# Performance work log

Measured on AMD Instinct MI355X. Metric: run time of the kernel, lower is better.

## Reference

```python
import jax, jax.numpy as jnp
import numpy as np

B, N, C = 8, 1024, 1024
H = 16
D = C // H  # head_dim = 64


def apply_rope(t, cos, sin):
    # t: (B,H,N,D), cos/sin: (N, D//2). Interleaved-pair RoPE
    # (matches repeat_interleave(2) + stack(-y2,y1) in the torch code).
    tr = t.reshape(*t.shape[:-1], D // 2, 2)
    t1, t2 = tr[..., 0], tr[..., 1]
    o1 = t1 * cos - t2 * sin
    o2 = t2 * cos + t1 * sin
    return jnp.stack((o1, o2), axis=-1).reshape(t.shape)


def setup_inputs() -> dict:
    key = jax.random.key(0)
    k1, k2, k3, k4 = jax.random.split(key, 4)
    s = 0.02
    x = jax.random.normal(k1, (B, N, C), dtype=jnp.float32)
    w_qkv = jax.random.normal(k2, (C, 3 * C), dtype=jnp.float32) * s  # qkv_bias=False
    w_proj = jax.random.normal(k3, (C, C), dtype=jnp.float32) * s
    b_proj = jax.random.normal(k4, (C,), dtype=jnp.float32) * s
    return {"x": x, "w_qkv": w_qkv, "w_proj": w_proj, "b_proj": b_proj}


def reference(x, w_qkv, w_proj, b_proj):
    # QKV projection: (B,N,3C) -> (3,B,H,N,D)
    qkv = (x @ w_qkv).reshape(B, N, 3, H, D).transpose(2, 0, 3, 1, 4)
    q, k, v = qkv[0], qkv[1], qkv[2]

    # RoPE tables: pos = arange(N) (mask=None, no cls/registers)
    pos = jnp.arange(N, dtype=jnp.float32)
    omega = 1.0 / (10000.0 ** (jnp.arange(D // 2, dtype=jnp.float32) / (D / 2.0)))
    freq = pos[:, None] * omega  # (N, D//2)
    cos, sin = jnp.cos(freq), jnp.sin(freq)

    q = apply_rope(q, cos, sin)
    k = apply_rope(k, cos, sin)

    # Scaled dot-product attention (non-causal, no dropout in eval)
    scale = 1.0 / jnp.sqrt(jnp.float32(D))
    scores = jnp.einsum('bhqd,bhkd->bhqk', q, k) * scale
    attn = jax.nn.softmax(scores, axis=-1)
    out = jnp.einsum('bhqk,bhkd->bhqd', attn, v)

    # Merge heads + output projection
    out = out.transpose(0, 2, 1, 3).reshape(B, N, C)
    return out @ w_proj + b_proj
```

## Files before the change

kernel.cpp:

```cpp
#include <hip/hip_runtime.h>
#include <hip/hip_bf16.h>
#include <math.h>

#define Bsz  8
#define Nseq 1024
#define Cdim 1024
#define Hh   16
#define Dd   64

typedef short short8 __attribute__((ext_vector_type(8)));
typedef float floatx4 __attribute__((ext_vector_type(4)));

__device__ __forceinline__ unsigned short f2bf(float f) {
    __hip_bfloat16 h = __float2bfloat16(f);
    return __builtin_bit_cast(unsigned short, h);
}
__device__ __forceinline__ float b2f(unsigned short u) {
    return __uint_as_float(((unsigned)u) << 16);
}

__device__ __forceinline__ void async16(const void* g, void* l) {
    __builtin_amdgcn_global_load_lds(
        (const __attribute__((address_space(1))) unsigned int*)g,
        (__attribute__((address_space(3))) unsigned int*)l, 16, 0, 0);
}

__device__ __forceinline__ unsigned pack_bf16(float lo, float hi) {
    unsigned ulo = __float_as_uint(lo) + 0x8000u;
    unsigned uhi = __float_as_uint(hi) + 0x8000u;
    return __builtin_amdgcn_perm(uhi, ulo, 0x07060302);
}

__global__ __launch_bounds__(256) void prep(
    const float* __restrict__ x, const float* __restrict__ w_qkv,
    const float* __restrict__ w_proj,
    unsigned short* __restrict__ xb, unsigned short* __restrict__ wqkvt,
    unsigned short* __restrict__ wprojt, float2* __restrict__ rope)
{
    __shared__ float T[64][65];
    const int blk = blockIdx.x;
    const int tid = threadIdx.x;

    if (blk < 8192) {
        int i = blk * 256 + tid;
        float4 v = ((const float4*)x)[i];
        ushort4 u;
        u.x = f2bf(v.x); u.y = f2bf(v.y); u.z = f2bf(v.z); u.w = f2bf(v.w);
        ((ushort4*)xb)[i] = u;
        return;
    }
    if (blk < 9216) {
        const float* in;
        unsigned short* out;
        int R = 1024, Ccols, c0, r0;
        if (blk < 8960) {
            int b2 = blk - 8192;
            in = w_qkv; out = wqkvt; Ccols = 3072;
            c0 = (b2 % 48) * 64; r0 = (b2 / 48) * 64;
        } else {
            int b2 = blk - 8960;
            in = w_proj; out = wprojt; Ccols = 1024;
            c0 = (b2 % 16) * 64; r0 = (b2 / 16) * 64;
        }
        for (int i = tid; i < 4096; i += 256) {
            int r = i >> 6, c = i & 63;
            T[r][c] = in[(size_t)(r0 + r) * Ccols + c0 + c];
        }
        __syncthreads();
        for (int i = tid; i < 4096; i += 256) {
            int rr = i >> 6, cc = i & 63;
            out[(size_t)(c0 + rr) * R + r0 + cc] = f2bf(T[cc][rr]);
        }
        return;
    }
    {
        int i = (blk - 9216) * 256 + tid;
        int n = i >> 5, p = i & 31;
        float omega = __expf(-(float)p * 0.2878231366242557f);
        float sv, cv;
        sincosf((float)n * omega, &sv, &cv);
        rope[i] = make_float2(cv, sv);
    }
}

template <int MODE>
__global__ __launch_bounds__(256) void gemm_bf16(
    const unsigned short* __restrict__ A, const unsigned short* __restrict__ Bt,
    const float* __restrict__ bias, const float2* __restrict__ rope,
    unsigned short* __restrict__ qb, unsigned short* __restrict__ kb,
    unsigned short* __restrict__ vtb, float* __restrict__ out)
{
    const int K = 1024;
    __shared__ short SM[2][128][64];
    const int tid  = threadIdx.x;
    const int wave = tid >> 6, lane = tid & 63;
    const int ml = lane & 15, quad = lane >> 4;
    const int wm = wave >> 1, wn = wave & 1;
    const int bm = blockIdx.y * 128, bn = blockIdx.x * 128;

    const int lr     = lane >> 3;
    const int lchunk = ((lane & 7) ^ lr) * 8;

    floatx4 acc[4][4] = {};

    for (int k0 = 0; k0 < K; k0 += 64) {
        #pragma unroll
        for (int t = 0; t < 4; ++t) {
            int r8  = (wave * 4 + t) * 8;
            int row = r8 + lr;
            async16(A  + (size_t)(bm + row) * K + k0 + lchunk, &SM[0][r8][0]);
            async16(Bt + (size_t)(bn + row) * K + k0 + lchunk, &SM[1][r8][0]);
        }
        __syncthreads();

        #pragma unroll
        for (int ks = 0; ks < 2; ++ks) {
            const int sl = ((ks * 4 + quad) ^ (ml & 7)) * 8;
            short8 araw[4], braw[4];
            #pragma unroll
            for (int mi = 0; mi < 4; ++mi)
                araw[mi] = *(const short8*)&SM[0][wm * 64 + mi * 16 + ml][sl];
            #pragma unroll
            for (int ni = 0; ni < 4; ++ni)
                braw[ni] = *(const short8*)&SM[1][wn * 64 + ni * 16 + ml][sl];
            #pragma unroll
            for (int mi = 0; mi < 4; ++mi)
                #pragma unroll
                for (int ni = 0; ni < 4; ++ni)
                    acc[mi][ni] = __builtin_amdgcn_mfma_f32_16x16x32_bf16(
                        araw[mi], braw[ni], acc[mi][ni], 0, 0, 0);
        }
        __syncthreads();
    }

    if (MODE == 0) {
        const int region = bn >> 10;
        const int b = bm >> 10;
        if (region < 2) {
            float2* Rs = (float2*)&SM[0][0][0];
            #pragma unroll
            for (int t = 0; t < 16; ++t) {
                int idx = t * 256 + tid;
                Rs[idx] = rope[(size_t)((bm + (idx >> 5)) & 1023) * 32 + (idx & 31)];
            }
            __syncthreads();
            unsigned short* dst = (region == 0) ? qb : kb;
            const float scale = (region == 0) ? 0.125f : 1.f;
            const float sgn = (ml & 1) ? 1.f : -1.f;
            #pragma unroll
            for (int ni = 0; ni < 4; ++ni) {
                int col = bn + wn * 64 + ni * 16 + ml;
                int jj = col & 1023;
                int h = jj >> 6, d = jj & 63;
                int p = d >> 1;
                #pragma unroll
                for (int mi = 0; mi < 4; ++mi)
                    #pragma unroll
                    for (int r = 0; r < 4; ++r) {
                        int rl = wm * 64 + mi * 16 + quad * 4 + r;
                        int n  = (bm + rl) & 1023;
                        float val = acc[mi][ni][r];
                        float partner = __shfl_xor(val, 1);
                        float2 cs = Rs[rl * 32 + p];
                        dst[(((size_t)(b * Hh + h)) * Nseq + n) * Dd + d] =
                            f2bf((val * cs.x + sgn * partner * cs.y) * scale);
                    }
            }
        } else {
            short* T = &SM[0][0][0];
            const int n0 = bm & 1023;
            #pragma unroll
            for (int hw = 0; hw < 2; ++hw) {
                if (hw) __syncthreads();
                if (wn == hw) {
                    #pragma unroll
                    for (int ni = 0; ni < 4; ++ni) {
                        int dcol = ni * 16 + ml;
                        #pragma unroll
                        for (int mi = 0; mi < 4; ++mi)
                            #pragma unroll
                            for (int r = 0; r < 4; ++r) {
                                int rl = wm * 64 + mi * 16 + quad * 4 + r;
                                T[dcol * 132 + rl] = (short)f2bf(acc[mi][ni][r]);
                            }
                    }
                }
                __syncthreads();
                int h = ((bn & 1023) >> 6) + hw;
                #pragma unroll
                for (int t = 0; t < 8; ++t) {
                    int idx4 = t * 256 + tid;
                    int d = idx4 >> 5, seg = idx4 & 31;
                    ushort4 v4 = *(const ushort4*)&T[d * 132 + seg * 4];
                    *(ushort4*)(vtb + (((size_t)(b * Hh + h)) * Dd + d) * Nseq
                                + n0 + seg * 4) = v4;
                }
            }
        }
    } else {
        #pragma unroll
        for (int ni = 0; ni < 4; ++ni) {
            int col = bn + wn * 64 + ni * 16 + ml;
            float bv = bias[col];
            #pragma unroll
            for (int mi = 0; mi < 4; ++mi)
                #pragma unroll
                for (int r = 0; r < 4; ++r) {
                    int row = bm + wm * 64 + mi * 16 + quad * 4 + r;
                    out[(size_t)row * 1024 + col] = acc[mi][ni][r] + bv;
                }
        }
    }
}

__global__ __launch_bounds__(256) void attn_flash_mfma(
    const unsigned short* __restrict__ qb, const unsigned short* __restrict__ kb,
    const unsigned short* __restrict__ vt, unsigned short* __restrict__ ao)
{
    const int bh  = blockIdx.x;
    const int qt  = blockIdx.y;
    const int tid = threadIdx.x;
    const int wave = tid >> 6, lane = tid & 63;
    const int ml = lane & 15, quad = lane >> 4;
    const int lr = lane >> 3;
    const int lc = ((lane & 7) ^ lr) * 8;

    __shared__ short Qs[128][64];
    __shared__ short Ks[64][64];
    __shared__ short Vs[64][64];
    __shared__ short Ps[4][32][72];

    const size_t hbase = (size_t)bh * (Nseq * Dd);
    const size_t vbase = (size_t)bh * 64;
    const int q0 = qt * 128;
    const int wq = wave * 32;
    const int wk = wave * 16;

    #pragma unroll
    for (int t = 0; t < 4; ++t)
        async16(qb + hbase + (size_t)(q0 + wq + t * 8 + lr) * 64 + lc, &Qs[wq + t * 8][0]);
    async16(kb + hbase + (size_t)(wk + lr) * 64 + lc,     &Ks[wk][0]);
    async16(kb + hbase + (size_t)(wk + 8 + lr) * 64 + lc, &Ks[wk + 8][0]);
    __syncthreads();

    short8 qfr[2][2];
    #pragma unroll
    for (int ks = 0; ks < 2; ++ks) {
        const int sl = ((ks * 4 + quad) ^ (ml & 7)) * 8;
        qfr[ks][0] = *(const short8*)&Qs[wq + ml][sl];
        qfr[ks][1] = *(const short8*)&Qs[wq + 16 + ml][sl];
    }

    float l0 = 0.f, l1 = 0.f;
    floatx4 o[2][4] = {};

    for (int kt = 0; kt < 16; ++kt) {
        const int k0r = kt * 64;
        async16(vt + (vbase + wk + lr) * Nseq + k0r + lc,     &Vs[wk][0]);
        async16(vt + (vbase + wk + 8 + lr) * Nseq + k0r + lc, &Vs[wk + 8][0]);

        floatx4 st[2][4] = {};
        #pragma unroll
        for (int ks = 0; ks < 2; ++ks) {
            const int sl = ((ks * 4 + quad) ^ (ml & 7)) * 8;
            #pragma unroll
            for (int kbk = 0; kbk < 4; ++kbk) {
                short8 kf = *(const short8*)&Ks[kbk * 16 + ml][sl];
                st[0][kbk] = __builtin_amdgcn_mfma_f32_16x16x32_bf16(kf, qfr[ks][0], st[0][kbk], 0, 0, 0);
                st[1][kbk] = __builtin_amdgcn_mfma_f32_16x16x32_bf16(kf, qfr[ks][1], st[1][kbk], 0, 0, 0);
            }
        }

        #pragma unroll
        for (int qg = 0; qg < 2; ++qg) {
            float lacc = 0.f;
            #pragma unroll
            for (int kbk = 0; kbk < 4; ++kbk) {
                float e0 = __expf(st[qg][kbk][0]);
                float e1 = __expf(st[qg][kbk][1]);
                float e2 = __expf(st[qg][kbk][2]);
                float e3 = __expf(st[qg][kbk][3]);
                lacc += (e0 + e1) + (e2 + e3);
                uint2 pk;
                pk.x = pack_bf16(e0, e1);
                pk.y = pack_bf16(e2, e3);
                *(uint2*)&Ps[wave][qg * 16 + ml][kbk * 16 + quad * 4] = pk;
            }
            if (qg == 0) l0 += lacc; else l1 += lacc;
        }
        __syncthreads();

        if (kt < 15) {
            const int k1r = k0r + 64;
            async16(kb + hbase + (size_t)(k1r + wk + lr) * 64 + lc,     &Ks[wk][0]);
            async16(kb + hbase + (size_t)(k1r + wk + 8 + lr) * 64 + lc, &Ks[wk + 8][0]);
        }

        #pragma unroll
        for (int ks = 0; ks < 2; ++ks) {
            const int sl = ((ks * 4 + quad) ^ (ml & 7)) * 8;
            short8 pf0 = *(const short8*)&Ps[wave][ml][ks * 32 + quad * 8];
            short8 pf1 = *(const short8*)&Ps[wave][16 + ml][ks * 32 + quad * 8];
            #pragma unroll
            for (int nt = 0; nt < 4; ++nt) {
                short8 vf = *(const short8*)&Vs[nt * 16 + ml][sl];
                o[0][nt] = __builtin_amdgcn_mfma_f32_16x16x32_bf16(pf0, vf, o[0][nt], 0, 0, 0);
                o[1][nt] = __builtin_amdgcn_mfma_f32_16x16x32_bf16(pf1, vf, o[1][nt], 0, 0, 0);
            }
        }
        if (kt < 15)
            __syncthreads();
    }

    l0 += __shfl_xor(l0, 16);
    l0 += __shfl_xor(l0, 32);
    l1 += __shfl_xor(l1, 16);
    l1 += __shfl_xor(l1, 32);

    const int b = bh >> 4, h = bh & 15;
    #pragma unroll
    for (int qg = 0; qg < 2; ++qg) {
        float lsrc = (qg == 0) ? l0 : l1;
        #pragma unroll
        for (int r = 0; r < 4; ++r) {
            float lq = __shfl(lsrc, quad * 4 + r);
            float inv = 1.f / lq;
            int q = q0 + wq + qg * 16 + quad * 4 + r;
            size_t rowbase = ((size_t)(b * Nseq + q)) * Cdim + h * Dd;
            #pragma unroll
            for (int nt = 0; nt < 4; ++nt)
                ao[rowbase + nt * 16 + ml] = f2bf(o[qg][nt][r] * inv);
        }
    }
}

extern "C" void kernel_launch(void* const* d_in, const int* in_sizes, int n_in,
                              void* d_out, int out_size, void* d_ws, size_t ws_size,
                              hipStream_t stream) {
    const float* x      = (const float*)d_in[0];
    const float* w_qkv  = (const float*)d_in[1];
    const float* w_proj = (const float*)d_in[2];
    const float* b_proj = (const float*)d_in[3];
    float* out = (float*)d_out;

    const size_t M8 = (size_t)8 * 1024 * 1024;
    unsigned short* qb     = (unsigned short*)d_ws;
    unsigned short* kb     = qb + M8;
    unsigned short* vt     = kb + M8;
    unsigned short* xb     = vt + M8;
    unsigned short* wqkvt  = xb + M8;
    unsigned short* wprojt = wqkvt + 3 * 1024 * 1024;
    float2*         rope   = (float2*)(wprojt + 1024 * 1024);
    unsigned short* aob    = xb;

    prep<<<9344, 256, 0, stream>>>(x, w_qkv, w_proj, xb, wqkvt, wprojt, rope);

    gemm_bf16<0><<<dim3(24, 64), 256, 0, stream>>>(xb, wqkvt, nullptr, rope,
                                                   qb, kb, vt, nullptr);

    attn_flash_mfma<<<dim3(128, 8), 256, 0, stream>>>(qb, kb, vt, aob);

    gemm_bf16<1><<<dim3(8, 64), 256, 0, stream>>>(aob, wprojt, b_proj, nullptr,
                                                  nullptr, nullptr, nullptr, out);
}
```

Before: 241.4 us.

## Replace 128x128 GEMM with double-buffered 256x256 tile, 8-wave pipelined kernel

Both bf16 GEMMs now use 256x256 output tiles computed by 512 threads (8 waves). Each k-step is split into four sub-steps, with async global-to-LDS loads into a second buffer overlapping the MFMA work, explicit vmcnt waits, barriers and s_setprio around the MFMA blocks. The larger tile raises operand reuse and the prefetch hides memory latency that the old load-sync-compute loop exposed. In exchange it uses 128KB of LDS and more registers, and the grid becomes small (384 blocks for QKV, 128 for the output projection), which may leave CUs idle on the proj GEMM.

```diff
diff --git a/kernel.cpp b/kernel.cpp
--- a/kernel.cpp
+++ b/kernel.cpp
@@ -14,9 +14,6 @@
 __device__ __forceinline__ unsigned short f2bf(float f) {
     __hip_bfloat16 h = __float2bfloat16(f);
     return __builtin_bit_cast(unsigned short, h);
-}
-__device__ __forceinline__ float b2f(unsigned short u) {
-    return __uint_as_float(((unsigned)u) << 16);
 }
 
 __device__ __forceinline__ void async16(const void* g, void* l) {
@@ -83,132 +80,212 @@
     }
 }
 
+__device__ __forceinline__ void load_a4(short8 ar[4][2], const short* buf,
+                                        int rowbase, int ml, int quad) {
+    #pragma unroll
+    for (int mi = 0; mi < 4; ++mi)
+        #pragma unroll
+        for (int ks = 0; ks < 2; ++ks) {
+            int sl = ((ks * 4 + quad) ^ (ml & 7)) * 8;
+            ar[mi][ks] = *(const short8*)&buf[(rowbase + mi * 16 + ml) * 64 + sl];
+        }
+}
+__device__ __forceinline__ void load_b2(short8 br[2][2], const short* buf,
+                                        int rowbase, int ml, int quad) {
+    #pragma unroll
+    for (int ni = 0; ni < 2; ++ni)
+        #pragma unroll
+        for (int ks = 0; ks < 2; ++ks) {
+            int sl = ((ks * 4 + quad) ^ (ml & 7)) * 8;
+            br[ni][ks] = *(const short8*)&buf[(rowbase + ni * 16 + ml) * 64 + sl];
+        }
+}
+__device__ __forceinline__ void mma16(floatx4 acc[4][2], const short8 ar[4][2],
+                                      const short8 br[2][2]) {
+    #pragma unroll
+    for (int ks = 0; ks < 2; ++ks)
+        #pragma unroll
+        for (int mi = 0; mi < 4; ++mi)
+            #pragma unroll
+            for (int ni = 0; ni < 2; ++ni)
+                acc[mi][ni] = __builtin_amdgcn_mfma_f32_16x16x32_bf16(
+                    ar[mi][ks], br[ni][ks], acc[mi][ni], 0, 0, 0);
+}
+__device__ __forceinline__ void stage_half(const unsigned short* g, short* dst,
+                                           int half, int k0, int wave, int lr,
+                                           int lchunk) {
+    #pragma unroll
+    for (int rr = 0; rr < 2; ++rr) {
+        int row = half * 128 + rr * 64 + wave * 8;
+        async16(g + (size_t)(row + lr) * 1024 + k0 + lchunk, dst + row * 64);
+    }
+}
+
+#define GTILE(CUR, T, S12, S34, VM1, VM4S)                                   \
+{                                                                            \
+                                                     \
+    load_a4(ar, Ab[CUR], wm * 64, ml, quad);                                 \
+    load_b2(br[0], Bb[CUR], wn * 32, ml, quad);                              \
+    if (S12) stage_half(Ag, Ab[1 - (CUR)], 1, ((T) + 1) * 64, wave, lr, lchunk); \
+    asm volatile("s_waitcnt vmcnt(" #VM1 ")" ::: "memory");                  \
+    __builtin_amdgcn_s_barrier();                                            \
+    asm volatile("s_waitcnt lgkmcnt(0)" ::: "memory");                       \
+    __builtin_amdgcn_s_setprio(1);                                           \
+    mma16(acc[0][0], ar, br[0]);                                             \
+    __builtin_amdgcn_s_setprio(0);                                           \
+    __builtin_amdgcn_s_barrier();                                            \
+    asm volatile("" ::: "memory");                                           \
+                                                     \
+    load_b2(br[1], Bb[CUR], 128 + wn * 32, ml, quad);                        \
+    if (S12) stage_half(Bg, Bb[1 - (CUR)], 1, ((T) + 1) * 64, wave, lr, lchunk); \
+    __builtin_amdgcn_s_barrier();                                            \
+    asm volatile("s_waitcnt lgkmcnt(0)" ::: "memory");                       \
+    __builtin_amdgcn_s_setprio(1);                                           \
+    mma16(acc[0][1], ar, br[1]);                                             \
+    __builtin_amdgcn_s_setprio(0);                                           \
+    __builtin_amdgcn_s_barrier();                                            \
+    asm volatile("" ::: "memory");                                           \
+                                                     \
+    load_a4(ar, Ab[CUR], 128 + wm * 64, ml, quad);                           \
+    if (S34) stage_half(Ag, Ab[CUR], 0, ((T) + 2) * 64, wave, lr, lchunk);   \
+    __builtin_amdgcn_s_barrier();                                            \
+    asm volatile("s_waitcnt lgkmcnt(0)" ::: "memory");                       \
+    __builtin_amdgcn_s_setprio(1);                                           \
+    mma16(acc[1][0], ar, br[0]);                                             \
+    __builtin_amdgcn_s_setprio(0);                                           \
+    __builtin_amdgcn_s_barrier();                                            \
+    asm volatile("" ::: "memory");                                           \
+                  \
+    if (S34) stage_half(Bg, Bb[CUR], 0, ((T) + 2) * 64, wave, lr, lchunk);   \
+    VM4S;                                                                    \
+    __builtin_amdgcn_s_barrier();                                            \
+    __builtin_amdgcn_s_setprio(1);                                           \
+    mma16(acc[1][1], ar, br[1]);                                             \
+    __builtin_amdgcn_s_setprio(0);                                           \
+    __builtin_amdgcn_s_barrier();                                            \
+    asm volatile("" ::: "memory");                                           \
+}
+#define VMW(n) asm volatile("s_waitcnt vmcnt(" #n ")" ::: "memory")
+
 template <int MODE>
-__global__ __launch_bounds__(256) void gemm_bf16(
+__global__ __launch_bounds__(512, 2) void gemm256(
     const unsigned short* __restrict__ A, const unsigned short* __restrict__ Bt,
     const float* __restrict__ bias, const float2* __restrict__ rope,
     unsigned short* __restrict__ qb, unsigned short* __restrict__ kb,
     unsigned short* __restrict__ vtb, float* __restrict__ out)
 {
-    const int K = 1024;
-    __shared__ short SM[2][128][64];
+    __shared__ __attribute__((aligned(16))) short SM[65536];
     const int tid  = threadIdx.x;
     const int wave = tid >> 6, lane = tid & 63;
     const int ml = lane & 15, quad = lane >> 4;
-    const int wm = wave >> 1, wn = wave & 1;
-    const int bm = blockIdx.y * 128, bn = blockIdx.x * 128;
-
     const int lr     = lane >> 3;
     const int lchunk = ((lane & 7) ^ lr) * 8;
-
-    floatx4 acc[4][4] = {};
-
-    for (int k0 = 0; k0 < K; k0 += 64) {
-        #pragma unroll
-        for (int t = 0; t < 4; ++t) {
-            int r8  = (wave * 4 + t) * 8;
-            int row = r8 + lr;
-            async16(A  + (size_t)(bm + row) * K + k0 + lchunk, &SM[0][r8][0]);
-            async16(Bt + (size_t)(bn + row) * K + k0 + lchunk, &SM[1][r8][0]);
-        }
+    const int wm = wave >> 2, wn = wave & 3;
+    const int bm = blockIdx.y * 256, bn = blockIdx.x * 256;
+
+    const unsigned short* Ag = A  + (size_t)bm * 1024;
+    const unsigned short* Bg = Bt + (size_t)bn * 1024;
+    short* const Ab[2] = { SM,         SM + 16384 };
+    short* const Bb[2] = { SM + 32768, SM + 49152 };
+
+    floatx4 acc[2][2][4][2] = {};
+    short8 ar[4][2], br[2][2][2];
+
+    stage_half(Ag, Ab[0], 0,  0, wave, lr, lchunk);
+    stage_half(Bg, Bb[0], 0,  0, wave, lr, lchunk);
+    stage_half(Ag, Ab[0], 1,  0, wave, lr, lchunk);
+    stage_half(Bg, Bb[0], 1,  0, wave, lr, lchunk);
+    stage_half(Ag, Ab[1], 0, 64, wave, lr, lchunk);
+    stage_half(Bg, Bb[1], 0, 64, wave, lr, lchunk);
+    asm volatile("s_waitcnt vmcnt(8)" ::: "memory");
+    __builtin_amdgcn_s_barrier();
+    asm volatile("" ::: "memory");
+
+    for (int t = 0; t < 14; t += 2) {
+        GTILE(0, t,     1, 1, 6, VMW(8));
+        GTILE(1, t + 1, 1, 1, 6, VMW(8));
+    }
+    GTILE(0, 14, 1, 0, 6, VMW(4));
+    GTILE(1, 15, 0, 0, 0, (void)0);
+
+    if (MODE == 1) {
+        #pragma unroll
+        for (int nh = 0; nh < 2; ++nh)
+            #pragma unroll
+            for (int ni = 0; ni < 2; ++ni) {
+                int col = bn + nh * 128 + wn * 32 + ni * 16 + ml;
+                float bv = bias[col];
+                #pragma unroll
+                for (int mh = 0; mh < 2; ++mh)
+                    #pragma unroll
+                    for (int mi = 0; mi < 4; ++mi)
+                        #pragma unroll
+                        for (int r = 0; r < 4; ++r) {
+                            int row = bm + mh * 128 + wm * 64 + mi * 16 + quad * 4 + r;
+                            out[(size_t)row * 1024 + col] = acc[mh][nh][mi][ni][r] + bv;
+                        }
+            }
+        return;
+    }
+
+    const int region = bn >> 10;
+    const int b  = bm >> 10;
+    const int n0 = bm & 1023;
+    if (region < 2) {
+        float2* Rs = (float2*)SM;
+        for (int i = tid; i < 8192; i += 512)
+            Rs[i] = rope[(size_t)(n0 + (i >> 5)) * 32 + (i & 31)];
         __syncthreads();
-
-        #pragma unroll
-        for (int ks = 0; ks < 2; ++ks) {
-            const int sl = ((ks * 4 + quad) ^ (ml & 7)) * 8;
-            short8 araw[4], braw[4];
-            #pragma unroll
-            for (int mi = 0; mi < 4; ++mi)
-                araw[mi] = *(const short8*)&SM[0][wm * 64 + mi * 16 + ml][sl];
-            #pragma unroll
-            for (int ni = 0; ni < 4; ++ni)
-                braw[ni] = *(const short8*)&SM[1][wn * 64 + ni * 16 + ml][sl];
-            #pragma unroll
-            for (int mi = 0; mi < 4; ++mi)
+        unsigned short* dst = (region == 0) ? qb : kb;
+        const float scale = (region == 0) ? 0.125f : 1.f;
+        const float sgn = (ml & 1) ? 1.f : -1.f;
+        #pragma unroll
+        for (int nh = 0; nh < 2; ++nh)
+            #pragma unroll
+            for (int ni = 0; ni < 2; ++ni) {
+                int col = (bn & 1023) + nh * 128 + wn * 32 + ni * 16 + ml;
+                int h = col >> 6, d = col & 63, p = d >> 1;
                 #pragma unroll
-                for (int ni = 0; ni < 4; ++ni)
-                    acc[mi][ni] = __builtin_amdgcn_mfma_f32_16x16x32_bf16(
-                        araw[mi], braw[ni], acc[mi][ni], 0, 0, 0);
-        }
-        __syncthreads();
-    }
-
-    if (MODE == 0) {
-        const int region = bn >> 10;
-        const int b = bm >> 10;
-        if (region < 2) {
-            float2* Rs = (float2*)&SM[0][0][0];
-            #pragma unroll
-            for (int t = 0; t < 16; ++t) {
-                int idx = t * 256 + tid;
-                Rs[idx] = rope[(size_t)((bm + (idx >> 5)) & 1023) * 32 + (idx & 31)];
-            }
-            __syncthreads();
-            unsigned short* dst = (region == 0) ? qb : kb;
-            const float scale = (region == 0) ? 0.125f : 1.f;
-            const float sgn = (ml & 1) ? 1.f : -1.f;
-            #pragma unroll
-            for (int ni = 0; ni < 4; ++ni) {
-                int col = bn + wn * 64 + ni * 16 + ml;
-                int jj = col & 1023;
-                int h = jj >> 6, d = jj & 63;
-                int p = d >> 1;
+                for (int mh = 0; mh < 2; ++mh)
+                    #pragma unroll
+                    for (int mi = 0; mi < 4; ++mi)
+                        #pragma unroll
+                        for (int r = 0; r < 4; ++r) {
+                            int rl = mh * 128 + wm * 64 + mi * 16 + quad * 4 + r;
+                            float val = acc[mh][nh][mi][ni][r];
+                            float partner = __shfl_xor(val, 1);
+                            float2 cs = Rs[rl * 32 + p];
+                            dst[(((size_t)(b * Hh + h)) * Nseq + n0 + rl) * Dd + d] =
+                                f2bf((val * cs.x + sgn * partner * cs.y) * scale);
+                        }
+            }
+    } else {
+        short* T = SM;
+        const int hb = (bn & 1023) >> 6;
+        #pragma unroll
+        for (int mh = 0; mh < 2; ++mh) {
+            if (mh) __syncthreads();
+            #pragma unroll
+            for (int nh = 0; nh < 2; ++nh)
                 #pragma unroll
-                for (int mi = 0; mi < 4; ++mi)
+                for (int ni = 0; ni < 2; ++ni) {
+                    int c = nh * 128 + wn * 32 + ni * 16 + ml;
                     #pragma unroll
-                    for (int r = 0; r < 4; ++r) {
-                        int rl = wm * 64 + mi * 16 + quad * 4 + r;
-                        int n  = (bm + rl) & 1023;
-                        float val = acc[mi][ni][r];
-                        float partner = __shfl_xor(val, 1);
-                        float2 cs = Rs[rl * 32 + p];
-                        dst[(((size_t)(b * Hh + h)) * Nseq + n) * Dd + d] =
-                            f2bf((val * cs.x + sgn * partner * cs.y) * scale);
-                    }
-            }
-        } else {
-            short* T = &SM[0][0][0];
-            const int n0 = bm & 1023;
-            #pragma unroll
-            for (int hw = 0; hw < 2; ++hw) {
-                if (hw) __syncthreads();
-                if (wn == hw) {
-                    #pragma unroll
-                    for (int ni = 0; ni < 4; ++ni) {
-                        int dcol = ni * 16 + ml;
-                        #pragma unroll
-                        for (int mi = 0; mi < 4; ++mi)
-                            #pragma unroll
-                            for (int r = 0; r < 4; ++r) {
-                                int rl = wm * 64 + mi * 16 + quad * 4 + r;
-                                T[dcol * 132 + rl] = (short)f2bf(acc[mi][ni][r]);
-                            }
+                    for (int mi = 0; mi < 4; ++mi) {
+                        uint2 pk;
+                        pk.x = pack_bf16(acc[mh][nh][mi][ni][0], acc[mh][nh][mi][ni][1]);
+                        pk.y = pack_bf16(acc[mh][nh][mi][ni][2], acc[mh][nh][mi][ni][3]);
+                        *(uint2*)&T[c * 136 + wm * 64 + mi * 16 + quad * 4] = pk;
                     }
                 }
-                __syncthreads();
-                int h = ((bn & 1023) >> 6) + hw;
-                #pragma unroll
-                for (int t = 0; t < 8; ++t) {
-                    int idx4 = t * 256 + tid;
-                    int d = idx4 >> 5, seg = idx4 & 31;
-                    ushort4 v4 = *(const ushort4*)&T[d * 132 + seg * 4];
-                    *(ushort4*)(vtb + (((size_t)(b * Hh + h)) * Dd + d) * Nseq
-                                + n0 + seg * 4) = v4;
-                }
-            }
-        }
-    } else {
-        #pragma unroll
-        for (int ni = 0; ni < 4; ++ni) {
-            int col = bn + wn * 64 + ni * 16 + ml;
-            float bv = bias[col];
-            #pragma unroll
-            for (int mi = 0; mi < 4; ++mi)
-                #pragma unroll
-                for (int r = 0; r < 4; ++r) {
-                    int row = bm + wm * 64 + mi * 16 + quad * 4 + r;
-                    out[(size_t)row * 1024 + col] = acc[mi][ni][r] + bv;
-                }
+            __syncthreads();
+            for (int i = tid; i < 8192; i += 512) {
+                int c = i >> 5, seg = i & 31;
+                ushort4 v4 = *(const ushort4*)&T[c * 136 + seg * 4];
+                int h = hb + (c >> 6), d = c & 63;
+                *(ushort4*)(vtb + (((size_t)(b * Hh + h)) * Dd + d) * Nseq
+                            + n0 + mh * 128 + seg * 4) = v4;
+            }
         }
     }
 }
@@ -355,11 +432,11 @@
 
     prep<<<9344, 256, 0, stream>>>(x, w_qkv, w_proj, xb, wqkvt, wprojt, rope);
 
-    gemm_bf16<0><<<dim3(24, 64), 256, 0, stream>>>(xb, wqkvt, nullptr, rope,
-                                                   qb, kb, vt, nullptr);
+    gemm256<0><<<dim3(12, 32), 512, 0, stream>>>(xb, wqkvt, nullptr, rope,
+                                                 qb, kb, vt, nullptr);
 
     attn_flash_mfma<<<dim3(128, 8), 256, 0, stream>>>(qb, kb, vt, aob);
 
-    gemm_bf16<1><<<dim3(8, 64), 256, 0, stream>>>(aob, wprojt, b_proj, nullptr,
-                                                  nullptr, nullptr, nullptr, out);
-}
+    gemm256<1><<<dim3(4, 32), 512, 0, stream>>>(aob, wprojt, b_proj, nullptr,
+                                                nullptr, nullptr, nullptr, out);
+}
```

Result: slower. 266.2 us (+10.3%).
